# Optimization experiments

Hardware: AMD Instinct MI355X
Metric: run time of the kernel (lower is better)

## Reference

```python
import jax, jax.numpy as jnp
import numpy as np

EPS = 1e-6

def _ln(x, g, b):
    mu = jnp.mean(x, -1, keepdims=True)
    var = jnp.mean((x - mu) ** 2, -1, keepdims=True)
    return (x - mu) / jnp.sqrt(var + EPS) * g + b

def _attn(q, k, v, nh, mask=None):
    B, Lq, H = q.shape
    Lk = k.shape[1]
    dh = H // nh
    q = q.reshape(B, Lq, nh, dh).transpose(0, 2, 1, 3)
    k = k.reshape(B, Lk, nh, dh).transpose(0, 2, 1, 3)
    v = v.reshape(B, Lk, nh, dh).transpose(0, 2, 1, 3)
    s = jnp.einsum('bhqd,bhkd->bhqk', q, k) * (1.0 / np.float32(np.sqrt(dh)))
    if mask is not None:
        s = jnp.where(mask, jnp.float32(-1e30), s)
    a = jax.nn.softmax(s, axis=-1)
    o = jnp.einsum('bhqk,bhkd->bhqd', a, v)
    return o.transpose(0, 2, 1, 3).reshape(B, Lq, H)

def _forward(byte_seq, patch_boundaries, emb, g_ln1_g, g_ln1_b, g_wqkv, g_bqkv, g_wo, g_bo,
             g_ln2_g, g_ln2_b, g_w1, g_b1, g_w2, g_b2, fn_g, fn_b,
             ca_ln_g, ca_ln_b, ca_wqkv, ca_bqkv, ca_wo, ca_bo, head_w, head_b,
             n_heads=16, ca_heads=8):
    B, S = byte_seq.shape
    P = patch_boundaries.shape[1]
    H = emb.shape[1]
    x = emb[byte_seq]  # [B,S,H] byte embeddings (local encoder)
    # ragged patch pooling: patch id of byte i = #boundaries <= i (BabylonIndex patches)
    pos = jnp.arange(S)
    pid = jax.vmap(lambda bd: jnp.searchsorted(bd, pos, side='right'))(patch_boundaries)
    pid = jnp.clip(pid, 0, P - 1)
    seg = lambda vals, ids: jax.ops.segment_sum(vals, ids, num_segments=P)
    sums = jax.vmap(seg)(x, pid)                                  # [B,P,H]
    cnts = jax.vmap(seg)(jnp.ones((B, S), x.dtype), pid)          # [B,P]
    patches = sums / jnp.maximum(cnts, 1.0)[..., None]            # mean-pooled patch reps
    causal = jnp.triu(jnp.ones((P, P), bool), 1)
    def layer(h, p):
        l1g, l1b, wqkv, bqkv, wo, bo, l2g, l2b, w1, b1, w2, b2 = p
        n = _ln(h, l1g, l1b)
        q, k, v = jnp.split(n @ wqkv + bqkv, 3, axis=-1)
        h = h + _attn(q, k, v, n_heads, causal) @ wo + bo
        n2 = _ln(h, l2g, l2b)
        h = h + jax.nn.gelu(n2 @ w1 + b1, approximate=False) @ w2 + b2
        return h, None
    patches, _ = jax.lax.scan(layer, patches, (g_ln1_g, g_ln1_b, g_wqkv, g_bqkv, g_wo, g_bo,
                                               g_ln2_g, g_ln2_b, g_w1, g_b1, g_w2, g_b2))
    patches = _ln(patches, fn_g, fn_b)  # GlobalLatentTransformer.final_norm
    # cross attention: byte queries attend to global patch representations
    qn = _ln(x, ca_ln_g, ca_ln_b)
    kvn = _ln(patches, ca_ln_g, ca_ln_b)
    q = qn @ ca_wqkv[:, :H] + ca_bqkv[:H]
    k = kvn @ ca_wqkv[:, H:2 * H] + ca_bqkv[H:2 * H]
    v = kvn @ ca_wqkv[:, 2 * H:] + ca_bqkv[2 * H:]
    h = x + _attn(q, k, v, ca_heads) @ ca_wo + ca_bo
    return h @ head_w + head_b  # [B,S,256] next-byte logits

def setup_inputs() -> dict:
    key = jax.random.key(0)
    ks = jax.random.split(key, 16)
    B, S, P, H, L, V = 2, 4096, 256, 1024, 4, 256
    std = 0.02
    d = {}
    d['byte_seq'] = jax.random.randint(ks[0], (B, S), 0, V, dtype=jnp.int32)
    d['patch_boundaries'] = jnp.sort(jax.random.randint(ks[1], (B, P), 1, S, dtype=jnp.int32), axis=-1)
    d['emb'] = jax.random.normal(ks[2], (V, H), jnp.float32) * std
    d['g_ln1_g'] = jnp.ones((L, H), jnp.float32)
    d['g_ln1_b'] = jnp.zeros((L, H), jnp.float32)
    d['g_wqkv'] = jax.random.normal(ks[3], (L, H, 3 * H), jnp.float32) * std
    d['g_bqkv'] = jnp.zeros((L, 3 * H), jnp.float32)
    d['g_wo'] = jax.random.normal(ks[4], (L, H, H), jnp.float32) * std
    d['g_bo'] = jnp.zeros((L, H), jnp.float32)
    d['g_ln2_g'] = jnp.ones((L, H), jnp.float32)
    d['g_ln2_b'] = jnp.zeros((L, H), jnp.float32)
    d['g_w1'] = jax.random.normal(ks[5], (L, H, 4 * H), jnp.float32) * std
    d['g_b1'] = jnp.zeros((L, 4 * H), jnp.float32)
    d['g_w2'] = jax.random.normal(ks[6], (L, 4 * H, H), jnp.float32) * std
    d['g_b2'] = jnp.zeros((L, H), jnp.float32)
    d['fn_g'] = jnp.ones((H,), jnp.float32)
    d['fn_b'] = jnp.zeros((H,), jnp.float32)
    d['ca_ln_g'] = jnp.ones((H,), jnp.float32)
    d['ca_ln_b'] = jnp.zeros((H,), jnp.float32)
    d['ca_wqkv'] = jax.random.normal(ks[7], (H, 3 * H), jnp.float32) * std
    d['ca_bqkv'] = jnp.zeros((3 * H,), jnp.float32)
    d['ca_wo'] = jax.random.normal(ks[8], (H, H), jnp.float32) * std
    d['ca_bo'] = jnp.zeros((H,), jnp.float32)
    d['head_w'] = jax.random.normal(ks[9], (H, V), jnp.float32) * std
    d['head_b'] = jnp.zeros((V,), jnp.float32)
    return d

def reference(byte_seq, patch_boundaries, emb, g_ln1_g, g_ln1_b, g_wqkv, g_bqkv, g_wo, g_bo,
              g_ln2_g, g_ln2_b, g_w1, g_b1, g_w2, g_b2, fn_g, fn_b,
              ca_ln_g, ca_ln_b, ca_wqkv, ca_bqkv, ca_wo, ca_bo, head_w, head_b):
    return _forward(byte_seq, patch_boundaries, emb, g_ln1_g, g_ln1_b, g_wqkv, g_bqkv, g_wo, g_bo,
                    g_ln2_g, g_ln2_b, g_w1, g_b1, g_w2, g_b2, fn_g, fn_b,
                    ca_ln_g, ca_ln_b, ca_wqkv, ca_bqkv, ca_wo, ca_bo, head_w, head_b)
```

## Files before the change

### kernel.cpp

```cpp
#include <hip/hip_runtime.h>
#include <hip/hip_bf16.h>
#include <math.h>

#define Hdim 1024
#define Bsz  2
#define Slen 4096
#define Pn   256
#define NLAY 4

typedef __attribute__((ext_vector_type(8))) __bf16 bfrag;
typedef __attribute__((ext_vector_type(4))) float  f32x4;

__device__ __forceinline__ float gelu_exact(float x) {
  return 0.5f * x * (1.0f + erff(x * 0.70710678118654752f));
}
__device__ __forceinline__ short f2b(float x) {
  __hip_bfloat16 h = __float2bfloat16(x);
  return *reinterpret_cast<short*>(&h);
}
__device__ __forceinline__ void gload16(const short* g, short* l) {
  __builtin_amdgcn_global_load_lds(
      (const __attribute__((address_space(1))) unsigned int*)g,
      (__attribute__((address_space(3))) unsigned int*)l, 16, 0, 0);
}
__device__ __forceinline__ void xcd_remap(int& bx, int& by) {
  int nwg = gridDim.x * gridDim.y;
  int bid = blockIdx.y * gridDim.x + blockIdx.x;
  int wg = (bid & 7) * (nwg >> 3) + (bid >> 3);
  bx = wg % gridDim.x;
  by = wg / gridDim.x;
}

__global__ void embed_ln_kernel(const int* __restrict__ seq, const float* __restrict__ emb,
                                const float* __restrict__ g, const float* __restrict__ bvec,
                                float* __restrict__ x, short* __restrict__ qn) {
  int row = blockIdx.x;
  int tid = threadIdx.x;
  int tok = seq[row];
  float4 v = *(const float4*)(emb + (size_t)tok * Hdim + tid * 4);
  *(float4*)(x + (size_t)row * Hdim + tid * 4) = v;
  float s  = v.x + v.y + v.z + v.w;
  float ss = v.x * v.x + v.y * v.y + v.z * v.z + v.w * v.w;
#pragma unroll
  for (int off = 32; off; off >>= 1) { s += __shfl_xor(s, off); ss += __shfl_xor(ss, off); }
  __shared__ float rs[4], rss[4];
  int wid = tid >> 6;
  if ((tid & 63) == 0) { rs[wid] = s; rss[wid] = ss; }
  __syncthreads();
  float tot  = rs[0] + rs[1] + rs[2] + rs[3];
  float tot2 = rss[0] + rss[1] + rss[2] + rss[3];
  float mu = tot * (1.0f / Hdim);
  float var = tot2 * (1.0f / Hdim) - mu * mu;
  float rstd = rsqrtf(var + 1e-6f);
  float4 gg = *(const float4*)(g + tid * 4);
  float4 bb = *(const float4*)(bvec + tid * 4);
  short4 o;
  o.x = f2b((v.x - mu) * rstd * gg.x + bb.x);
  o.y = f2b((v.y - mu) * rstd * gg.y + bb.y);
  o.z = f2b((v.z - mu) * rstd * gg.z + bb.z);
  o.w = f2b((v.w - mu) * rstd * gg.w + bb.w);
  *(short4*)(qn + (size_t)row * Hdim + tid * 4) = o;
}

__global__ void pid_kernel(const int* __restrict__ bounds, int* __restrict__ pid) {
  int i = blockIdx.x * 256 + threadIdx.x;
  int b = i >> 12;
  int s = i & (Slen - 1);
  const int* bd = bounds + b * Pn;
  int lo = 0, hi = Pn;
  while (lo < hi) { int m = (lo + hi) >> 1; if (bd[m] <= s) lo = m + 1; else hi = m; }
  pid[i] = min(lo, Pn - 1);
}

__global__ void pool_kernel(const float* __restrict__ x, const int* __restrict__ pid,
                            float* __restrict__ patches) {
  int bp = blockIdx.x;
  int b = bp >> 8;
  int p = bp & (Pn - 1);
  const int* pv = pid + b * Slen;
  int lo = 0, hi = Slen;
  while (lo < hi) { int m = (lo + hi) >> 1; if (pv[m] < p) lo = m + 1; else hi = m; }
  int start = lo;
  lo = 0; hi = Slen;
  while (lo < hi) { int m = (lo + hi) >> 1; if (pv[m] < p + 1) lo = m + 1; else hi = m; }
  int end = lo;
  int tid = threadIdx.x;
  float4 acc = {0.f, 0.f, 0.f, 0.f};
  for (int s = start; s < end; ++s) {
    float4 xv = *(const float4*)(x + ((size_t)(b * Slen + s)) * Hdim + tid * 4);
    acc.x += xv.x; acc.y += xv.y; acc.z += xv.z; acc.w += xv.w;
  }
  float cnt = (float)(end - start);
  float r = 1.0f / fmaxf(cnt, 1.0f);
  float4 o = {acc.x * r, acc.y * r, acc.z * r, acc.w * r};
  *(float4*)(patches + (size_t)bp * Hdim + tid * 4) = o;
}

template<int OBF>
__global__ void ln_kernel(const float* __restrict__ in, const float* __restrict__ g,
                          const float* __restrict__ bvec, void* __restrict__ outv) {
  int row = blockIdx.x;
  int tid = threadIdx.x;
  const float* xr = in + (size_t)row * Hdim;
  float4 v = *(const float4*)(xr + tid * 4);
  float s  = v.x + v.y + v.z + v.w;
  float ss = v.x * v.x + v.y * v.y + v.z * v.z + v.w * v.w;
#pragma unroll
  for (int off = 32; off; off >>= 1) { s += __shfl_xor(s, off); ss += __shfl_xor(ss, off); }
  __shared__ float rs[4], rss[4];
  int wid = tid >> 6;
  if ((tid & 63) == 0) { rs[wid] = s; rss[wid] = ss; }
  __syncthreads();
  float tot  = rs[0] + rs[1] + rs[2] + rs[3];
  float tot2 = rss[0] + rss[1] + rss[2] + rss[3];
  float mu = tot * (1.0f / Hdim);
  float var = tot2 * (1.0f / Hdim) - mu * mu;
  float rstd = rsqrtf(var + 1e-6f);
  float4 gg = *(const float4*)(g + tid * 4);
  float4 bb = *(const float4*)(bvec + tid * 4);
  float4 r;
  r.x = (v.x - mu) * rstd * gg.x + bb.x;
  r.y = (v.y - mu) * rstd * gg.y + bb.y;
  r.z = (v.z - mu) * rstd * gg.z + bb.z;
  r.w = (v.w - mu) * rstd * gg.w + bb.w;
  if (OBF) {
    short4 o; o.x = f2b(r.x); o.y = f2b(r.y); o.z = f2b(r.z); o.w = f2b(r.w);
    *(short4*)((short*)outv + (size_t)row * Hdim + tid * 4) = o;
  } else {
    *(float4*)((float*)outv + (size_t)row * Hdim + tid * 4) = r;
  }
}

__global__ void wconv_kernel(const float* __restrict__ in, short* __restrict__ out,
                             int ldin, int K, size_t in_lstride, size_t out_lstride) {
  int z = blockIdx.z;
  const float* src = in + (size_t)z * in_lstride;
  short* dst = out + (size_t)z * out_lstride;
  int n0 = blockIdx.x * 32, k0 = blockIdx.y * 32;
  int tx = threadIdx.x & 31, ty = threadIdx.x >> 5;
  __shared__ float t[32][33];
#pragma unroll
  for (int i = 0; i < 4; i++)
    t[ty + 8 * i][tx] = src[(size_t)(k0 + ty + 8 * i) * ldin + n0 + tx];
  __syncthreads();
#pragma unroll
  for (int i = 0; i < 4; i++)
    dst[(size_t)(n0 + ty + 8 * i) * K + k0 + tx] = f2b(t[tx][ty + 8 * i]);
}

__global__ void vt_kernel(const float* __restrict__ in, short* __restrict__ out) {
  int bh = blockIdx.z; int h = bh & 7; int b = bh >> 3;
  int kk0 = blockIdx.x * 32, d0 = blockIdx.y * 32;
  int tx = threadIdx.x & 31, ty = threadIdx.x >> 5;
  __shared__ float t[32][33];
  const float* src = in + (size_t)b * Pn * Hdim + h * 128;
#pragma unroll
  for (int i = 0; i < 4; i++)
    t[ty + 8 * i][tx] = src[(size_t)(kk0 + ty + 8 * i) * Hdim + d0 + tx];
  __syncthreads();
  short* dst = out + (size_t)bh * 128 * 256;
#pragma unroll
  for (int i = 0; i < 4; i++)
    dst[(size_t)(d0 + ty + 8 * i) * 256 + kk0 + tx] = f2b(t[tx][ty + 8 * i]);
}

__global__ void vtg_kernel(const short* __restrict__ qkvb, short* __restrict__ out) {
  int bh = blockIdx.z; int h = bh & 15; int b = bh >> 4;
  int kk0 = blockIdx.x * 32, d0 = blockIdx.y * 32;
  int tx = threadIdx.x & 31, ty = threadIdx.x >> 5;
  __shared__ short t[32][33];
  const short* src = qkvb + (size_t)b * Pn * 3072 + 2048 + h * 64;
#pragma unroll
  for (int i = 0; i < 4; i++)
    t[ty + 8 * i][tx] = src[(size_t)(kk0 + ty + 8 * i) * 3072 + d0 + tx];
  __syncthreads();
  short* dst = out + (size_t)bh * 64 * 256;
#pragma unroll
  for (int i = 0; i < 4; i++)
    dst[(size_t)(d0 + ty + 8 * i) * 256 + kk0 + tx] = t[tx][ty + 8 * i];
}

template<int EPI, int OBF, int SWZ>
__launch_bounds__(256)
__global__ void gemm_bf16(const short* __restrict__ A, const short* __restrict__ Bt,
                          const float* __restrict__ bias, const float* __restrict__ res,
                          void* __restrict__ Cv, int ldc, int K) {
  __shared__ short As[128 * 32];
  __shared__ short Bs[128 * 32];
  int tid = threadIdx.x;
  int bx = blockIdx.x, by = blockIdx.y;
  if (SWZ) xcd_remap(bx, by);
  int n0 = bx * 128, m0 = by * 128;
  int lr = tid >> 2;
  int lc = (tid & 3) * 8;
  int wid = tid >> 6, lane = tid & 63;
  int wm = (wid & 1) * 64, wn = (wid >> 1) * 64;
  int quad = lane >> 4, l16 = lane & 15;
  f32x4 acc[4][4];
#pragma unroll
  for (int i = 0; i < 4; i++)
#pragma unroll
    for (int j = 0; j < 4; j++) acc[i][j] = (f32x4){0.f, 0.f, 0.f, 0.f};

  const short* ga0 = A + (size_t)(m0 + lr) * K + lc;
  const short* ga1 = A + (size_t)(m0 + lr + 64) * K + lc;
  const short* gb0 = Bt + (size_t)(n0 + lr) * K + lc;
  const short* gb1 = Bt + (size_t)(n0 + lr + 64) * K + lc;
  short* la0 = As + tid * 8;
  short* la1 = As + 2048 + tid * 8;
  short* lb0 = Bs + tid * 8;
  short* lb1 = Bs + 2048 + tid * 8;

  for (int k0 = 0; k0 < K; k0 += 32) {
    __syncthreads();
    gload16(ga0 + k0, la0);
    gload16(ga1 + k0, la1);
    gload16(gb0 + k0, lb0);
    gload16(gb1 + k0, lb1);
    __syncthreads();
    bfrag af[4], bfv[4];
#pragma unroll
    for (int mi = 0; mi < 4; mi++)
      af[mi] = *reinterpret_cast<const bfrag*>(&As[(wm + mi * 16 + l16) * 32 + quad * 8]);
#pragma unroll
    for (int ni = 0; ni < 4; ni++)
      bfv[ni] = *reinterpret_cast<const bfrag*>(&Bs[(wn + ni * 16 + l16) * 32 + quad * 8]);
#pragma unroll
    for (int mi = 0; mi < 4; mi++)
#pragma unroll
      for (int ni = 0; ni < 4; ni++)
        acc[mi][ni] = __builtin_amdgcn_mfma_f32_16x16x32_bf16(af[mi], bfv[ni], acc[mi][ni], 0, 0, 0);
  }

#pragma unroll
  for (int mi = 0; mi < 4; mi++)
#pragma unroll
    for (int ni = 0; ni < 4; ni++) {
      int c = n0 + wn + ni * 16 + l16;
      float bsv = bias[c];
#pragma unroll
      for (int reg = 0; reg < 4; reg++) {
        int r = m0 + wm + mi * 16 + quad * 4 + reg;
        float v = acc[mi][ni][reg] + bsv;
        if (EPI == 1) v = gelu_exact(v);
        if (EPI == 2) v += res[(size_t)r * ldc + c];
        if (OBF) ((short*)Cv)[(size_t)r * ldc + c] = f2b(v);
        else     ((float*)Cv)[(size_t)r * ldc + c] = v;
      }
    }
}

template<int EPI, int OBF, int SWZ>
__launch_bounds__(256)
__global__ void gemm_bf16_64(const short* __restrict__ A, const short* __restrict__ Bt,
                             const float* __restrict__ bias, const float* __restrict__ res,
                             void* __restrict__ Cv, int ldc, int K) {
  __shared__ short As[64 * 32];
  __shared__ short Bs[64 * 32];
  int tid = threadIdx.x;
  int bx = blockIdx.x, by = blockIdx.y;
  if (SWZ) xcd_remap(bx, by);
  int n0 = bx * 64, m0 = by * 64;
  int lr = tid >> 2;
  int lc = (tid & 3) * 8;
  int wid = tid >> 6, lane = tid & 63;
  int wm = (wid & 1) * 32, wn = (wid >> 1) * 32;
  int quad = lane >> 4, l16 = lane & 15;
  f32x4 acc[2][2];
#pragma unroll
  for (int i = 0; i < 2; i++)
#pragma unroll
    for (int j = 0; j < 2; j++) acc[i][j] = (f32x4){0.f, 0.f, 0.f, 0.f};

  const short* ga = A + (size_t)(m0 + lr) * K + lc;
  const short* gb = Bt + (size_t)(n0 + lr) * K + lc;
  short* la = As + tid * 8;
  short* lb = Bs + tid * 8;

  for (int k0 = 0; k0 < K; k0 += 32) {
    __syncthreads();
    gload16(ga + k0, la);
    gload16(gb + k0, lb);
    __syncthreads();
    bfrag af[2], bfv[2];
#pragma unroll
    for (int mi = 0; mi < 2; mi++)
      af[mi] = *reinterpret_cast<const bfrag*>(&As[(wm + mi * 16 + l16) * 32 + quad * 8]);
#pragma unroll
    for (int ni = 0; ni < 2; ni++)
      bfv[ni] = *reinterpret_cast<const bfrag*>(&Bs[(wn + ni * 16 + l16) * 32 + quad * 8]);
#pragma unroll
    for (int mi = 0; mi < 2; mi++)
#pragma unroll
      for (int ni = 0; ni < 2; ni++)
        acc[mi][ni] = __builtin_amdgcn_mfma_f32_16x16x32_bf16(af[mi], bfv[ni], acc[mi][ni], 0, 0, 0);
  }

#pragma unroll
  for (int mi = 0; mi < 2; mi++)
#pragma unroll
    for (int ni = 0; ni < 2; ni++) {
      int c = n0 + wn + ni * 16 + l16;
      float bsv = bias[c];
#pragma unroll
      for (int reg = 0; reg < 4; reg++) {
        int r = m0 + wm + mi * 16 + quad * 4 + reg;
        float v = acc[mi][ni][reg] + bsv;
        if (EPI == 1) v = gelu_exact(v);
        if (EPI == 2) v += res[(size_t)r * ldc + c];
        if (OBF) ((short*)Cv)[(size_t)r * ldc + c] = f2b(v);
        else     ((float*)Cv)[(size_t)r * ldc + c] = v;
      }
    }
}

__launch_bounds__(256)
__global__ void gemm_splitk(const short* __restrict__ A, const short* __restrict__ Bt,
                            float* __restrict__ part, int K, int Ks) {
  __shared__ short As[64 * 32];
  __shared__ short Bs[64 * 32];
  int tid = threadIdx.x;
  int n0 = blockIdx.x * 64, m0 = blockIdx.y * 64, s = blockIdx.z;
  int kbase = s * Ks;
  int lr = tid >> 2;
  int lc = (tid & 3) * 8;
  int wid = tid >> 6, lane = tid & 63;
  int wm = (wid & 1) * 32, wn = (wid >> 1) * 32;
  int quad = lane >> 4, l16 = lane & 15;
  f32x4 acc[2][2];
#pragma unroll
  for (int i = 0; i < 2; i++)
#pragma unroll
    for (int j = 0; j < 2; j++) acc[i][j] = (f32x4){0.f, 0.f, 0.f, 0.f};

  const short* ga = A + (size_t)(m0 + lr) * K + lc;
  const short* gb = Bt + (size_t)(n0 + lr) * K + lc;
  short* la = As + tid * 8;
  short* lb = Bs + tid * 8;

  for (int k0 = kbase; k0 < kbase + Ks; k0 += 32) {
    __syncthreads();
    gload16(ga + k0, la);
    gload16(gb + k0, lb);
    __syncthreads();
    bfrag af[2], bfv[2];
#pragma unroll
    for (int mi = 0; mi < 2; mi++)
      af[mi] = *reinterpret_cast<const bfrag*>(&As[(wm + mi * 16 + l16) * 32 + quad * 8]);
#pragma unroll
    for (int ni = 0; ni < 2; ni++)
      bfv[ni] = *reinterpret_cast<const bfrag*>(&Bs[(wn + ni * 16 + l16) * 32 + quad * 8]);
#pragma unroll
    for (int mi = 0; mi < 2; mi++)
#pragma unroll
      for (int ni = 0; ni < 2; ni++)
        acc[mi][ni] = __builtin_amdgcn_mfma_f32_16x16x32_bf16(af[mi], bfv[ni], acc[mi][ni], 0, 0, 0);
  }

#pragma unroll
  for (int mi = 0; mi < 2; mi++)
#pragma unroll
    for (int ni = 0; ni < 2; ni++) {
      int c = n0 + wn + ni * 16 + l16;
#pragma unroll
      for (int reg = 0; reg < 4; reg++) {
        int r = m0 + wm + mi * 16 + quad * 4 + reg;
        part[(size_t)s * 524288 + (size_t)r * 1024 + c] = acc[mi][ni][reg];
      }
    }
}

__global__ void w2red_kernel(const float* __restrict__ part, const float* __restrict__ bias,
                             float* __restrict__ patches) {
  int i = (blockIdx.x * 256 + threadIdx.x) * 4;
  float4 v = *(const float4*)(part + i);
#pragma unroll
  for (int s = 1; s < 4; s++) {
    float4 p = *(const float4*)(part + (size_t)s * 524288 + i);
    v.x += p.x; v.y += p.y; v.z += p.z; v.w += p.w;
  }
  int c = i & 1023;
  float4 bv = *(const float4*)(bias + c);
  float4 rv = *(const float4*)(patches + i);
  v.x += bv.x + rv.x; v.y += bv.y + rv.y; v.z += bv.z + rv.z; v.w += bv.w + rv.w;
  *(float4*)(patches + i) = v;
}

__launch_bounds__(256)
__global__ void attn_global3(const short* __restrict__ qkvb, const short* __restrict__ vtg,
                             short* __restrict__ outp) {
  int qt = blockIdx.x;
  int bh = blockIdx.y; int h = bh & 15, b = bh >> 4;
  int tid = threadIdx.x;
  int wid = tid >> 6, lane = tid & 63;
  int quad = lane >> 4, l16 = lane & 15;
  int q0 = qt * 64 + wid * 16;
  __shared__ short KV[64 * 72];
  __shared__ short Pl[4][16][264];
  const short* qrow = qkvb + ((size_t)(b * Pn + q0 + l16)) * 3072 + h * 64 + quad * 8;
  bfrag qf[2];
#pragma unroll
  for (int kd = 0; kd < 2; kd++) qf[kd] = *(const bfrag*)(qrow + kd * 32);
  f32x4 sacc[16];
#pragma unroll
  for (int n = 0; n < 16; n++) sacc[n] = (f32x4){0.f, 0.f, 0.f, 0.f};
  int cr = tid >> 2, cc = (tid & 3) * 16;
#pragma unroll
  for (int kc = 0; kc < 4; kc++) {
    if (kc <= qt) {
      const short* ksrc = qkvb + ((size_t)(b * Pn + kc * 64 + cr)) * 3072 + 1024 + h * 64 + cc;
      int4 v0 = *(const int4*)(ksrc);
      int4 v1 = *(const int4*)(ksrc + 8);
      __syncthreads();
      *(int4*)&KV[cr * 72 + cc] = v0;
      *(int4*)&KV[cr * 72 + cc + 8] = v1;
      __syncthreads();
#pragma unroll
      for (int n = 0; n < 4; n++)
#pragma unroll
        for (int kd = 0; kd < 2; kd++) {
          bfrag kf = *(const bfrag*)&KV[(n * 16 + l16) * 72 + kd * 32 + quad * 8];
          sacc[kc * 4 + n] = __builtin_amdgcn_mfma_f32_16x16x32_bf16(qf[kd], kf, sacc[kc * 4 + n], 0, 0, 0);
        }
    }
  }
  int nfr = (qt + 1) * 4;
  const float scale = 0.125f;
  float mx[4] = {-1e30f, -1e30f, -1e30f, -1e30f};
#pragma unroll
  for (int n = 0; n < 16; n++) {
    if (n < nfr) {
      int col = n * 16 + l16;
#pragma unroll
      for (int r = 0; r < 4; r++)
        if (col <= q0 + quad * 4 + r) mx[r] = fmaxf(mx[r], sacc[n][r]);
    }
  }
#pragma unroll
  for (int off = 1; off < 16; off <<= 1)
#pragma unroll
    for (int r = 0; r < 4; r++) mx[r] = fmaxf(mx[r], __shfl_xor(mx[r], off));
  float ls[4] = {0.f, 0.f, 0.f, 0.f};
#pragma unroll
  for (int n = 0; n < 16; n++) {
    if (n < nfr) {
      int col = n * 16 + l16;
#pragma unroll
      for (int r = 0; r < 4; r++) {
        float p = (col <= q0 + quad * 4 + r) ? __expf((sacc[n][r] - mx[r]) * scale) : 0.f;
        Pl[wid][quad * 4 + r][col] = f2b(p);
        ls[r] += p;
      }
    }
  }
#pragma unroll
  for (int off = 1; off < 16; off <<= 1)
#pragma unroll
    for (int r = 0; r < 4; r++) ls[r] += __shfl_xor(ls[r], off);
  float rl[4];
#pragma unroll
  for (int r = 0; r < 4; r++) rl[r] = 1.0f / ls[r];

  f32x4 oacc[4];
#pragma unroll
  for (int n = 0; n < 4; n++) oacc[n] = (f32x4){0.f, 0.f, 0.f, 0.f};
#pragma unroll
  for (int kc = 0; kc < 4; kc++) {
    if (kc <= qt) {
      const short* vsrc = vtg + (size_t)bh * 64 * 256 + cr * 256 + kc * 64 + cc;
      int4 v0 = *(const int4*)(vsrc);
      int4 v1 = *(const int4*)(vsrc + 8);
      __syncthreads();
      *(int4*)&KV[cr * 72 + cc] = v0;
      *(int4*)&KV[cr * 72 + cc + 8] = v1;
      __syncthreads();
#pragma unroll
      for (int kk = 0; kk < 2; kk++) {
        bfrag pa = *(const bfrag*)&Pl[wid][l16][kc * 64 + kk * 32 + quad * 8];
#pragma unroll
        for (int n = 0; n < 4; n++) {
          bfrag vf = *(const bfrag*)&KV[(n * 16 + l16) * 72 + kk * 32 + quad * 8];
          oacc[n] = __builtin_amdgcn_mfma_f32_16x16x32_bf16(pa, vf, oacc[n], 0, 0, 0);
        }
      }
    }
  }
#pragma unroll
  for (int n = 0; n < 4; n++)
#pragma unroll
    for (int r = 0; r < 4; r++)
      outp[(size_t)(b * Pn + q0 + quad * 4 + r) * Hdim + h * 64 + n * 16 + l16] = f2b(oacc[n][r] * rl[r]);
}

__launch_bounds__(256)
__global__ void attn_cross4(const short* __restrict__ q, const short* __restrict__ k,
                            const short* __restrict__ vt, short* __restrict__ outp) {
  int bh = blockIdx.y; int h = bh & 7, b = bh >> 3;
  int tid = threadIdx.x;
  int wid = tid >> 6, lane = tid & 63;
  int quad = lane >> 4, l16 = lane & 15;
  int q0 = blockIdx.x * 64 + wid * 16;
  __shared__ short KV[9216];
  __shared__ short Pl[4][16][264];
  const short* qrow = q + ((size_t)(b * Slen + q0 + l16)) * Hdim + h * 128 + quad * 8;
  bfrag qf[4];
#pragma unroll
  for (int kd = 0; kd < 4; kd++) qf[kd] = *(const bfrag*)(qrow + kd * 32);
  f32x4 sacc[16];
#pragma unroll
  for (int n = 0; n < 16; n++) sacc[n] = (f32x4){0.f, 0.f, 0.f, 0.f};

  int cr4 = tid >> 2, cc4 = (tid & 3) * 32;
#pragma unroll
  for (int kc = 0; kc < 4; kc++) {
    const short* ksrc = k + ((size_t)(b * Pn + kc * 64 + cr4)) * Hdim + h * 128 + cc4;
    int4 v0 = *(const int4*)(ksrc);
    int4 v1 = *(const int4*)(ksrc + 8);
    int4 v2 = *(const int4*)(ksrc + 16);
    int4 v3 = *(const int4*)(ksrc + 24);
    __syncthreads();
    *(int4*)&KV[cr4 * 136 + cc4]      = v0;
    *(int4*)&KV[cr4 * 136 + cc4 + 8]  = v1;
    *(int4*)&KV[cr4 * 136 + cc4 + 16] = v2;
    *(int4*)&KV[cr4 * 136 + cc4 + 24] = v3;
    __syncthreads();
#pragma unroll
    for (int n = 0; n < 4; n++)
#pragma unroll
      for (int kd = 0; kd < 4; kd++) {
        bfrag kf = *(const bfrag*)&KV[(n * 16 + l16) * 136 + kd * 32 + quad * 8];
        sacc[kc * 4 + n] = __builtin_amdgcn_mfma_f32_16x16x32_bf16(qf[kd], kf, sacc[kc * 4 + n], 0, 0, 0);
      }
  }

  const float scale = 0.088388347648318447f;
  float mx[4] = {-1e30f, -1e30f, -1e30f, -1e30f};
#pragma unroll
  for (int n = 0; n < 16; n++)
#pragma unroll
    for (int r = 0; r < 4; r++) mx[r] = fmaxf(mx[r], sacc[n][r]);
#pragma unroll
  for (int off = 1; off < 16; off <<= 1)
#pragma unroll
    for (int r = 0; r < 4; r++) mx[r] = fmaxf(mx[r], __shfl_xor(mx[r], off));
  float ls[4] = {0.f, 0.f, 0.f, 0.f};
#pragma unroll
  for (int n = 0; n < 16; n++)
#pragma unroll
    for (int r = 0; r < 4; r++) {
      float p = __expf((sacc[n][r] - mx[r]) * scale);
      Pl[wid][quad * 4 + r][n * 16 + l16] = f2b(p);
      ls[r] += p;
    }
#pragma unroll
  for (int off = 1; off < 16; off <<= 1)
#pragma unroll
    for (int r = 0; r < 4; r++) ls[r] += __shfl_xor(ls[r], off);
  float rl[4];
#pragma unroll
  for (int r = 0; r < 4; r++) rl[r] = 1.0f / ls[r];

  f32x4 oacc[8];
#pragma unroll
  for (int n = 0; n < 8; n++) oacc[n] = (f32x4){0.f, 0.f, 0.f, 0.f};
  int cr2 = tid >> 1, cc2 = (tid & 1) * 32;
#pragma unroll
  for (int kc = 0; kc < 4; kc++) {
    const short* vsrc = vt + (size_t)bh * 32768 + cr2 * 256 + kc * 64 + cc2;
    int4 v0 = *(const int4*)(vsrc);
    int4 v1 = *(const int4*)(vsrc + 8);
    int4 v2 = *(const int4*)(vsrc + 16);
    int4 v3 = *(const int4*)(vsrc + 24);
    __syncthreads();
    *(int4*)&KV[cr2 * 72 + cc2]      = v0;
    *(int4*)&KV[cr2 * 72 + cc2 + 8]  = v1;
    *(int4*)&KV[cr2 * 72 + cc2 + 16] = v2;
    *(int4*)&KV[cr2 * 72 + cc2 + 24] = v3;
    __syncthreads();
#pragma unroll
    for (int kk = 0; kk < 2; kk++) {
      bfrag pa = *(const bfrag*)&Pl[wid][l16][kc * 64 + kk * 32 + quad * 8];
#pragma unroll
      for (int n = 0; n < 8; n++) {
        bfrag vf = *(const bfrag*)&KV[(n * 16 + l16) * 72 + kk * 32 + quad * 8];
        oacc[n] = __builtin_amdgcn_mfma_f32_16x16x32_bf16(pa, vf, oacc[n], 0, 0, 0);
      }
    }
  }
#pragma unroll
  for (int n = 0; n < 8; n++)
#pragma unroll
    for (int r = 0; r < 4; r++)
      outp[(size_t)(b * Slen + q0 + quad * 4 + r) * Hdim + h * 128 + n * 16 + l16] = f2b(oacc[n][r] * rl[r]);
}

extern "C" void kernel_launch(void* const* d_in, const int* in_sizes, int n_in,
                              void* d_out, int out_size, void* d_ws, size_t ws_size,
                              hipStream_t stream) {
  const int*   byte_seq = (const int*)d_in[0];
  const int*   pbound   = (const int*)d_in[1];
  const float* emb      = (const float*)d_in[2];
  const float* g_ln1_g  = (const float*)d_in[3];
  const float* g_ln1_b  = (const float*)d_in[4];
  const float* g_wqkv   = (const float*)d_in[5];
  const float* g_bqkv   = (const float*)d_in[6];
  const float* g_wo     = (const float*)d_in[7];
  const float* g_bo     = (const float*)d_in[8];
  const float* g_ln2_g  = (const float*)d_in[9];
  const float* g_ln2_b  = (const float*)d_in[10];
  const float* g_w1     = (const float*)d_in[11];
  const float* g_b1     = (const float*)d_in[12];
  const float* g_w2     = (const float*)d_in[13];
  const float* g_b2     = (const float*)d_in[14];
  const float* fn_g     = (const float*)d_in[15];
  const float* fn_b     = (const float*)d_in[16];
  const float* ca_ln_g  = (const float*)d_in[17];
  const float* ca_ln_b  = (const float*)d_in[18];
  const float* ca_wqkv  = (const float*)d_in[19];
  const float* ca_bqkv  = (const float*)d_in[20];
  const float* ca_wo    = (const float*)d_in[21];
  const float* ca_bo    = (const float*)d_in[22];
  const float* head_w   = (const float*)d_in[23];
  const float* head_b   = (const float*)d_in[24];
  float* out = (float*)d_out;

  float* x       = (float*)d_ws;
  float* patches = x + 8388608;
  float* vbuf    = patches + 524288;
  float* w2part  = vbuf + 524288;
  int*   pid     = (int*)(w2part + 2097152);
  short* nbuf    = (short*)(pid + 8192);
  short* attn_o  = nbuf + 524288;
  short* mid     = attn_o + 524288;
  short* qn      = mid + 2097152;
  short* qb      = qn + 8388608;
  short* xb      = qb + 8388608;
  short* kb      = xb + 8388608;
  short* vt      = kb + 524288;
  short* qkvb    = vt + 524288;
  short* vtg     = qkvb + 1572864;
  short* wqkv_t  = vtg + 524288;
  short* wo_t    = wqkv_t + 12582912;
  short* w1_t    = wo_t + 4194304;
  short* w2_t    = w1_t + 16777216;
  short* caq_t   = w2_t + 16777216;
  short* cak_t   = caq_t + 1048576;
  short* cav_t   = cak_t + 1048576;
  short* cawo_t  = cav_t + 1048576;
  short* head_t  = cawo_t + 1048576;
  short* caout   = qn;

  embed_ln_kernel<<<Bsz * Slen, 256, 0, stream>>>(byte_seq, emb, ca_ln_g, ca_ln_b, x, qn);
  pid_kernel<<<(Bsz * Slen) / 256, 256, 0, stream>>>(pbound, pid);
  pool_kernel<<<Bsz * Pn, 256, 0, stream>>>(x, pid, patches);

  wconv_kernel<<<dim3(96, 32, 4), 256, 0, stream>>>(g_wqkv, wqkv_t, 3072, 1024, 3145728, 3145728);
  wconv_kernel<<<dim3(32, 32, 4), 256, 0, stream>>>(g_wo, wo_t, 1024, 1024, 1048576, 1048576);
  wconv_kernel<<<dim3(128, 32, 4), 256, 0, stream>>>(g_w1, w1_t, 4096, 1024, 4194304, 4194304);
  wconv_kernel<<<dim3(32, 128, 4), 256, 0, stream>>>(g_w2, w2_t, 1024, 4096, 4194304, 4194304);
  wconv_kernel<<<dim3(32, 32, 3), 256, 0, stream>>>(ca_wqkv, caq_t, 3072, 1024, 1024, 1048576);
  wconv_kernel<<<dim3(32, 32, 1), 256, 0, stream>>>(ca_wo, cawo_t, 1024, 1024, 0, 0);
  wconv_kernel<<<dim3(8, 32, 1), 256, 0, stream>>>(head_w, head_t, 256, 1024, 0, 0);

  for (int l = 0; l < NLAY; ++l) {
    ln_kernel<1><<<Bsz * Pn, 256, 0, stream>>>(patches, g_ln1_g + l * Hdim, g_ln1_b + l * Hdim, nbuf);
    gemm_bf16_64<0, 1, 0><<<dim3(48, 8), 256, 0, stream>>>(
        nbuf, wqkv_t + (size_t)l * 3145728, g_bqkv + l * 3072, nullptr, qkvb, 3072, 1024);
    vtg_kernel<<<dim3(8, 2, 32), 256, 0, stream>>>(qkvb, vtg);
    attn_global3<<<dim3(4, 32), 256, 0, stream>>>(qkvb, vtg, attn_o);
    gemm_bf16_64<2, 0, 0><<<dim3(16, 8), 256, 0, stream>>>(
        attn_o, wo_t + (size_t)l * 1048576, g_bo + l * Hdim, patches, patches, 1024, 1024);
    ln_kernel<1><<<Bsz * Pn, 256, 0, stream>>>(patches, g_ln2_g + l * Hdim, g_ln2_b + l * Hdim, nbuf);
    gemm_bf16_64<1, 1, 0><<<dim3(64, 8), 256, 0, stream>>>(
        nbuf, w1_t + (size_t)l * 4194304, g_b1 + l * 4096, nullptr, mid, 4096, 1024);
    gemm_splitk<<<dim3(16, 8, 4), 256, 0, stream>>>(
        mid, w2_t + (size_t)l * 4194304, w2part, 4096, 1024);
    w2red_kernel<<<512, 256, 0, stream>>>(w2part, g_b2 + l * Hdim, patches);
  }

  ln_kernel<0><<<Bsz * Pn, 256, 0, stream>>>(patches, fn_g, fn_b, patches);
  ln_kernel<1><<<Bsz * Pn, 256, 0, stream>>>(patches, ca_ln_g, ca_ln_b, nbuf);

  gemm_bf16_64<0, 1, 0><<<dim3(16, 8), 256, 0, stream>>>(
      nbuf, cak_t, ca_bqkv + 1024, nullptr, kb, 1024, 1024);
  gemm_bf16_64<0, 0, 0><<<dim3(16, 8), 256, 0, stream>>>(
      nbuf, cav_t, ca_bqkv + 2048, nullptr, vbuf, 1024, 1024);
  vt_kernel<<<dim3(8, 4, 16), 256, 0, stream>>>(vbuf, vt);

  gemm_bf16<0, 1, 1><<<dim3(8, 64), 256, 0, stream>>>(
      qn, caq_t, ca_bqkv, nullptr, qb, 1024, 1024);

  attn_cross4<<<dim3(64, 16), 256, 0, stream>>>(qb, kb, vt, caout);

  gemm_bf16<2, 1, 1><<<dim3(8, 64), 256, 0, stream>>>(
      caout, cawo_t, ca_bo, x, xb, 1024, 1024);

  gemm_bf16_64<0, 0, 1><<<dim3(4, 128), 256, 0, stream>>>(
      xb, head_t, head_b, nullptr, out, 256, 1024);
}
```

Measured before the change: 831.9 us.

## Double-buffer GEMM LDS tiles with BK=64 and XOR-swizzled layout

All three bf16 GEMM kernels now use two LDS buffers with K-tile 64, prefetching the next tile via global_load_lds while MFMAs run on the current one. The LDS layout is XOR-swizzled per row to avoid bank conflicts on fragment reads, and there is now one barrier per 64-K step instead of two per 32-K step. In exchange, LDS use per block quadruples (64KB for the 128 tile), which may reduce occupancy, and K must be a multiple of 64.

Result: faster. 771.5 us (-7.3%).

```diff
diff --git a/kernel.cpp b/kernel.cpp
--- a/kernel.cpp
+++ b/kernel.cpp
@@ -185,14 +185,14 @@
 __global__ void gemm_bf16(const short* __restrict__ A, const short* __restrict__ Bt,
                           const float* __restrict__ bias, const float* __restrict__ res,
                           void* __restrict__ Cv, int ldc, int K) {
-  __shared__ short As[128 * 32];
-  __shared__ short Bs[128 * 32];
+  __shared__ short As[2][128 * 64];
+  __shared__ short Bs[2][128 * 64];
   int tid = threadIdx.x;
   int bx = blockIdx.x, by = blockIdx.y;
   if (SWZ) xcd_remap(bx, by);
   int n0 = bx * 128, m0 = by * 128;
-  int lr = tid >> 2;
-  int lc = (tid & 3) * 8;
+  int lr = tid >> 3;
+  int lc = (((tid & 7) ^ (lr & 7)) * 8);
   int wid = tid >> 6, lane = tid & 63;
   int wm = (wid & 1) * 64, wn = (wid >> 1) * 64;
   int quad = lane >> 4, l16 = lane & 15;
@@ -202,34 +202,54 @@
 #pragma unroll
     for (int j = 0; j < 4; j++) acc[i][j] = (f32x4){0.f, 0.f, 0.f, 0.f};
 
-  const short* ga0 = A + (size_t)(m0 + lr) * K + lc;
-  const short* ga1 = A + (size_t)(m0 + lr + 64) * K + lc;
-  const short* gb0 = Bt + (size_t)(n0 + lr) * K + lc;
-  const short* gb1 = Bt + (size_t)(n0 + lr + 64) * K + lc;
-  short* la0 = As + tid * 8;
-  short* la1 = As + 2048 + tid * 8;
-  short* lb0 = Bs + tid * 8;
-  short* lb1 = Bs + 2048 + tid * 8;
-
-  for (int k0 = 0; k0 < K; k0 += 32) {
-    __syncthreads();
-    gload16(ga0 + k0, la0);
-    gload16(ga1 + k0, la1);
-    gload16(gb0 + k0, lb0);
-    gload16(gb1 + k0, lb1);
-    __syncthreads();
-    bfrag af[4], bfv[4];
-#pragma unroll
-    for (int mi = 0; mi < 4; mi++)
-      af[mi] = *reinterpret_cast<const bfrag*>(&As[(wm + mi * 16 + l16) * 32 + quad * 8]);
-#pragma unroll
-    for (int ni = 0; ni < 4; ni++)
-      bfv[ni] = *reinterpret_cast<const bfrag*>(&Bs[(wn + ni * 16 + l16) * 32 + quad * 8]);
-#pragma unroll
-    for (int mi = 0; mi < 4; mi++)
-#pragma unroll
-      for (int ni = 0; ni < 4; ni++)
-        acc[mi][ni] = __builtin_amdgcn_mfma_f32_16x16x32_bf16(af[mi], bfv[ni], acc[mi][ni], 0, 0, 0);
+  const short* ga = A + (size_t)(m0 + lr) * K + lc;
+  const short* gb = Bt + (size_t)(n0 + lr) * K + lc;
+  short* la = &As[0][tid * 8];
+  short* lb = &Bs[0][tid * 8];
+
+#pragma unroll
+  for (int r = 0; r < 4; r++) {
+    gload16(ga + (size_t)(r * 32) * K, la + r * 2048);
+    gload16(gb + (size_t)(r * 32) * K, lb + r * 2048);
+  }
+  asm volatile("s_waitcnt vmcnt(0)" ::: "memory");
+  __builtin_amdgcn_s_barrier();
+
+  int NT = K >> 6;
+  for (int t = 0; t < NT; ++t) {
+    int cur = t & 1;
+    if (t + 1 < NT) {
+      int nb = (cur ^ 1) * 8192;
+      int k1 = (t + 1) << 6;
+#pragma unroll
+      for (int r = 0; r < 4; r++) {
+        gload16(ga + (size_t)(r * 32) * K + k1, la + nb + r * 2048);
+        gload16(gb + (size_t)(r * 32) * K + k1, lb + nb + r * 2048);
+      }
+    }
+#pragma unroll
+    for (int kk = 0; kk < 2; kk++) {
+      bfrag af[4], bfv[4];
+#pragma unroll
+      for (int mi = 0; mi < 4; mi++) {
+        int row = wm + mi * 16 + l16;
+        af[mi] = *reinterpret_cast<const bfrag*>(
+            &As[cur][row * 64 + (((kk * 4 + quad) ^ (row & 7)) * 8)]);
+      }
+#pragma unroll
+      for (int ni = 0; ni < 4; ni++) {
+        int row = wn + ni * 16 + l16;
+        bfv[ni] = *reinterpret_cast<const bfrag*>(
+            &Bs[cur][row * 64 + (((kk * 4 + quad) ^ (row & 7)) * 8)]);
+      }
+#pragma unroll
+      for (int mi = 0; mi < 4; mi++)
+#pragma unroll
+        for (int ni = 0; ni < 4; ni++)
+          acc[mi][ni] = __builtin_amdgcn_mfma_f32_16x16x32_bf16(af[mi], bfv[ni], acc[mi][ni], 0, 0, 0);
+    }
+    asm volatile("s_waitcnt vmcnt(0)" ::: "memory");
+    __builtin_amdgcn_s_barrier();
   }
 
 #pragma unroll
@@ -255,14 +275,14 @@
 __global__ void gemm_bf16_64(const short* __restrict__ A, const short* __restrict__ Bt,
                              const float* __restrict__ bias, const float* __restrict__ res,
                              void* __restrict__ Cv, int ldc, int K) {
-  __shared__ short As[64 * 32];
-  __shared__ short Bs[64 * 32];
+  __shared__ short As[2][64 * 64];
+  __shared__ short Bs[2][64 * 64];
   int tid = threadIdx.x;
   int bx = blockIdx.x, by = blockIdx.y;
   if (SWZ) xcd_remap(bx, by);
   int n0 = bx * 64, m0 = by * 64;
-  int lr = tid >> 2;
-  int lc = (tid & 3) * 8;
+  int lr = tid >> 3;
+  int lc = (((tid & 7) ^ (lr & 7)) * 8);
   int wid = tid >> 6, lane = tid & 63;
   int wm = (wid & 1) * 32, wn = (wid >> 1) * 32;
   int quad = lane >> 4, l16 = lane & 15;
@@ -274,26 +294,52 @@
 
   const short* ga = A + (size_t)(m0 + lr) * K + lc;
   const short* gb = Bt + (size_t)(n0 + lr) * K + lc;
-  short* la = As + tid * 8;
-  short* lb = Bs + tid * 8;
-
-  for (int k0 = 0; k0 < K; k0 += 32) {
-    __syncthreads();
-    gload16(ga + k0, la);
-    gload16(gb + k0, lb);
-    __syncthreads();
-    bfrag af[2], bfv[2];
-#pragma unroll
-    for (int mi = 0; mi < 2; mi++)
-      af[mi] = *reinterpret_cast<const bfrag*>(&As[(wm + mi * 16 + l16) * 32 + quad * 8]);
-#pragma unroll
-    for (int ni = 0; ni < 2; ni++)
-      bfv[ni] = *reinterpret_cast<const bfrag*>(&Bs[(wn + ni * 16 + l16) * 32 + quad * 8]);
-#pragma unroll
-    for (int mi = 0; mi < 2; mi++)
-#pragma unroll
-      for (int ni = 0; ni < 2; ni++)
-        acc[mi][ni] = __builtin_amdgcn_mfma_f32_16x16x32_bf16(af[mi], bfv[ni], acc[mi][ni], 0, 0, 0);
+  short* la = &As[0][tid * 8];
+  short* lb = &Bs[0][tid * 8];
+
+#pragma unroll
+  for (int r = 0; r < 2; r++) {
+    gload16(ga + (size_t)(r * 32) * K, la + r * 2048);
+    gload16(gb + (size_t)(r * 32) * K, lb + r * 2048);
+  }
+  asm volatile("s_waitcnt vmcnt(0)" ::: "memory");
+  __builtin_amdgcn_s_barrier();
+
+  int NT = K >> 6;
+  for (int t = 0; t < NT; ++t) {
+    int cur = t & 1;
+    if (t + 1 < NT) {
+      int nb = (cur ^ 1) * 4096;
+      int k1 = (t + 1) << 6;
+#pragma unroll
+      for (int r = 0; r < 2; r++) {
+        gload16(ga + (size_t)(r * 32) * K + k1, la + nb + r * 2048);
+        gload16(gb + (size_t)(r * 32) * K + k1, lb + nb + r * 2048);
+      }
+    }
+#pragma unroll
+    for (int kk = 0; kk < 2; kk++) {
+      bfrag af[2], bfv[2];
+#pragma unroll
+      for (int mi = 0; mi < 2; mi++) {
+        int row = wm + mi * 16 + l16;
+        af[mi] = *reinterpret_cast<const bfrag*>(
+            &As[cur][row * 64 + (((kk * 4 + quad) ^ (row & 7)) * 8)]);
+      }
+#pragma unroll
+      for (int ni = 0; ni < 2; ni++) {
+        int row = wn + ni * 16 + l16;
+        bfv[ni] = *reinterpret_cast<const bfrag*>(
+            &Bs[cur][row * 64 + (((kk * 4 + quad) ^ (row & 7)) * 8)]);
+      }
+#pragma unroll
+      for (int mi = 0; mi < 2; mi++)
+#pragma unroll
+        for (int ni = 0; ni < 2; ni++)
+          acc[mi][ni] = __builtin_amdgcn_mfma_f32_16x16x32_bf16(af[mi], bfv[ni], acc[mi][ni], 0, 0, 0);
+    }
+    asm volatile("s_waitcnt vmcnt(0)" ::: "memory");
+    __builtin_amdgcn_s_barrier();
   }
 
 #pragma unroll
@@ -317,13 +363,13 @@
 __launch_bounds__(256)
 __global__ void gemm_splitk(const short* __restrict__ A, const short* __restrict__ Bt,
                             float* __restrict__ part, int K, int Ks) {
-  __shared__ short As[64 * 32];
-  __shared__ short Bs[64 * 32];
+  __shared__ short As[2][64 * 64];
+  __shared__ short Bs[2][64 * 64];
   int tid = threadIdx.x;
   int n0 = blockIdx.x * 64, m0 = blockIdx.y * 64, s = blockIdx.z;
   int kbase = s * Ks;
-  int lr = tid >> 2;
-  int lc = (tid & 3) * 8;
+  int lr = tid >> 3;
+  int lc = (((tid & 7) ^ (lr & 7)) * 8);
   int wid = tid >> 6, lane = tid & 63;
   int wm = (wid & 1) * 32, wn = (wid >> 1) * 32;
   int quad = lane >> 4, l16 = lane & 15;
@@ -333,28 +379,54 @@
 #pragma unroll
     for (int j = 0; j < 2; j++) acc[i][j] = (f32x4){0.f, 0.f, 0.f, 0.f};
 
-  const short* ga = A + (size_t)(m0 + lr) * K + lc;
-  const short* gb = Bt + (size_t)(n0 + lr) * K + lc;
-  short* la = As + tid * 8;
-  short* lb = Bs + tid * 8;
-
-  for (int k0 = kbase; k0 < kbase + Ks; k0 += 32) {
-    __syncthreads();
-    gload16(ga + k0, la);
-    gload16(gb + k0, lb);
-    __syncthreads();
-    bfrag af[2], bfv[2];
-#pragma unroll
-    for (int mi = 0; mi < 2; mi++)
-      af[mi] = *reinterpret_cast<const bfrag*>(&As[(wm + mi * 16 + l16) * 32 + quad * 8]);
-#pragma unroll
-    for (int ni = 0; ni < 2; ni++)
-      bfv[ni] = *reinterpret_cast<const bfrag*>(&Bs[(wn + ni * 16 + l16) * 32 + quad * 8]);
-#pragma unroll
-    for (int mi = 0; mi < 2; mi++)
-#pragma unroll
-      for (int ni = 0; ni < 2; ni++)
-        acc[mi][ni] = __builtin_amdgcn_mfma_f32_16x16x32_bf16(af[mi], bfv[ni], acc[mi][ni], 0, 0, 0);
+  const short* ga = A + (size_t)(m0 + lr) * K + kbase + lc;
+  const short* gb = Bt + (size_t)(n0 + lr) * K + kbase + lc;
+  short* la = &As[0][tid * 8];
+  short* lb = &Bs[0][tid * 8];
+
+#pragma unroll
+  for (int r = 0; r < 2; r++) {
+    gload16(ga + (size_t)(r * 32) * K, la + r * 2048);
+    gload16(gb + (size_t)(r * 32) * K, lb + r * 2048);
+  }
+  asm volatile("s_waitcnt vmcnt(0)" ::: "memory");
+  __builtin_amdgcn_s_barrier();
+
+  int NT = Ks >> 6;
+  for (int t = 0; t < NT; ++t) {
+    int cur = t & 1;
+    if (t + 1 < NT) {
+      int nb = (cur ^ 1) * 4096;
+      int k1 = (t + 1) << 6;
+#pragma unroll
+      for (int r = 0; r < 2; r++) {
+        gload16(ga + (size_t)(r * 32) * K + k1, la + nb + r * 2048);
+        gload16(gb + (size_t)(r * 32) * K + k1, lb + nb + r * 2048);
+      }
+    }
+#pragma unroll
+    for (int kk = 0; kk < 2; kk++) {
+      bfrag af[2], bfv[2];
+#pragma unroll
+      for (int mi = 0; mi < 2; mi++) {
+        int row = wm + mi * 16 + l16;
+        af[mi] = *reinterpret_cast<const bfrag*>(
+            &As[cur][row * 64 + (((kk * 4 + quad) ^ (row & 7)) * 8)]);
+      }
+#pragma unroll
+      for (int ni = 0; ni < 2; ni++) {
+        int row = wn + ni * 16 + l16;
+        bfv[ni] = *reinterpret_cast<const bfrag*>(
+            &Bs[cur][row * 64 + (((kk * 4 + quad) ^ (row & 7)) * 8)]);
+      }
+#pragma unroll
+      for (int mi = 0; mi < 2; mi++)
+#pragma unroll
+        for (int ni = 0; ni < 2; ni++)
+          acc[mi][ni] = __builtin_amdgcn_mfma_f32_16x16x32_bf16(af[mi], bfv[ni], acc[mi][ni], 0, 0, 0);
+    }
+    asm volatile("s_waitcnt vmcnt(0)" ::: "memory");
+    __builtin_amdgcn_s_barrier();
   }
 
 #pragma unroll
```
